# Optimization experiments

Measured on AMD Instinct MI355X. Metric: run time of the kernel, lower is better.

Reference implementation:

```python
import jax, jax.numpy as jnp
import numpy as np

H, E, D, S, B = 16, 1024, 64, 2048, 4  # heads, emb, head_size, seq_len, batch

def setup_inputs() -> dict:
    key = jax.random.key(0)
    ks = jax.random.split(key, 9)
    sc_e = 1.0 / np.sqrt(E)
    sc_hd = 1.0 / np.sqrt(H * D)
    return {
        "x":  jax.random.normal(ks[0], (B, S, E), dtype=jnp.float32),
        # per-head q/k/v projection weights, stacked: [H, E, D]
        "Wq": jax.random.uniform(ks[1], (H, E, D), jnp.float32, -sc_e, sc_e),
        "Wk": jax.random.uniform(ks[2], (H, E, D), jnp.float32, -sc_e, sc_e),
        "Wv": jax.random.uniform(ks[3], (H, E, D), jnp.float32, -sc_e, sc_e),
        "bq": jax.random.uniform(ks[4], (H, D), jnp.float32, -sc_e, sc_e),
        "bk": jax.random.uniform(ks[5], (H, D), jnp.float32, -sc_e, sc_e),
        "bv": jax.random.uniform(ks[6], (H, D), jnp.float32, -sc_e, sc_e),
        # output projection: Linear(H*D -> E)
        "Wo": jax.random.uniform(ks[7], (H * D, E), jnp.float32, -sc_hd, sc_hd),
        "bo": jax.random.uniform(ks[8], (E,), jnp.float32, -sc_hd, sc_hd),
    }

def reference(x, Wq, Wk, Wv, bq, bk, bv, Wo, bo):
    b, s, e = x.shape
    # batched per-head projections: [B, H, S, D]
    q = jnp.einsum("bse,hed->bhsd", x, Wq) + bq[None, :, None, :]
    k = jnp.einsum("bse,hed->bhsd", x, Wk) + bk[None, :, None, :]
    v = jnp.einsum("bse,hed->bhsd", x, Wv) + bv[None, :, None, :]
    scale = 1.0 / jnp.sqrt(jnp.asarray(q.shape[-1], q.dtype))
    scores = jnp.einsum("bhqd,bhkd->bhqk", q, k) * scale  # [B,H,S,S]
    causal = jnp.tril(jnp.ones((s, s), dtype=bool))
    scores = jnp.where(causal[None, None], scores, jnp.asarray(-jnp.inf, scores.dtype))
    attn = jax.nn.softmax(scores, axis=-1)
    heads = jnp.einsum("bhqk,bhkd->bhqd", attn, v)  # [B,H,S,D]
    concat = heads.transpose(0, 2, 1, 3).reshape(b, s, -1)  # [B,S,H*D]
    return concat @ Wo + bo  # dropout is identity at inference
```

## Files before the change

### kernel.cpp

```cpp
#include <hip/hip_runtime.h>
#include <hip/hip_bf16.h>

#define H_ 16
#define E_ 1024
#define D_ 64
#define S_ 2048
#define B_ 4
#define M_ (B_ * S_)

typedef __bf16 bf16_t;
typedef __bf16 bf16x8 __attribute__((ext_vector_type(8)));
typedef __bf16 bf16x4 __attribute__((ext_vector_type(4)));
typedef float f32x4 __attribute__((ext_vector_type(4)));

typedef __attribute__((address_space(1))) unsigned int gu32;
typedef __attribute__((address_space(3))) unsigned int lu32;

__device__ __forceinline__ f32x4 mfma16(bf16x8 a, bf16x8 b, f32x4 c) {
  return __builtin_amdgcn_mfma_f32_16x16x32_bf16(a, b, c, 0, 0, 0);
}
__device__ __forceinline__ void gl2lds16(const bf16_t* g, bf16_t* l) {
  __builtin_amdgcn_global_load_lds((const gu32*)g, (lu32*)l, 16, 0, 0);
}

__global__ void detect_k(const unsigned short* __restrict__ x, int* __restrict__ flag) {
  __shared__ int cnt;
  if (threadIdx.x == 0) cnt = 0;
  __syncthreads();
  int hits = 0;
  for (int i = 0; i < 4; ++i) {
    unsigned short v = x[(threadIdx.x * 4 + i) * 2];
    int e = (v >> 7) & 0xFF;
    if (e >= 0xC0) hits++;
  }
  atomicAdd(&cnt, hits);
  __syncthreads();
  if (threadIdx.x == 0) { flag[0] = (cnt > 32) ? 1 : 0; flag[1] = 0; }
}

__global__ __launch_bounds__(256) void convert_x(
    const void* __restrict__ src, bf16_t* __restrict__ dst,
    const int* __restrict__ flag, long n) {
  long i = ((long)blockIdx.x * 256 + threadIdx.x) * 8;
  if (i >= n) return;
  bf16x8 v;
  if (*flag) {
    const float* s = (const float*)src;
    for (int j = 0; j < 8; ++j) v[j] = (bf16_t)s[i + j];
  } else {
    v = *(const bf16x8*)((const bf16_t*)src + i);
  }
  *(bf16x8*)(dst + i) = v;
}

__global__ __launch_bounds__(256) void transpose_k(
    const void* __restrict__ src_, bf16_t* __restrict__ dst,
    const int* __restrict__ flag, int K, int N, long sStride, long dStride) {
  __shared__ __align__(16) bf16_t tile[64][72];
  const int f32 = *flag;
  dst += (long)blockIdx.z * dStride;
  const int tk = blockIdx.x * 64, tn = blockIdx.y * 64;
  const int t = threadIdx.x;
  for (int i = 0; i < 2; ++i) {
    int c = t + i * 256;
    int r = c >> 3, col = (c & 7) * 8;
    if (f32) {
      const float* s = (const float*)src_ + (long)blockIdx.z * sStride;
      const float* p = &s[(long)(tk + r) * N + tn + col];
      for (int j = 0; j < 8; ++j) tile[r][col + j] = (bf16_t)p[j];
    } else {
      const bf16_t* s = (const bf16_t*)src_ + (long)blockIdx.z * sStride;
      *(bf16x8*)&tile[r][col] = *(const bf16x8*)&s[(long)(tk + r) * N + tn + col];
    }
  }
  __syncthreads();
  for (int i = 0; i < 2; ++i) {
    int c = t + i * 256;
    int r = c >> 3, col = (c & 7) * 8;
    bf16x8 v;
    for (int j = 0; j < 8; ++j) v[j] = tile[col + j][r];
    *(bf16x8*)&dst[(long)(tn + r) * K + tk + col] = v;
  }
}

__global__ __launch_bounds__(256) void transpose_qkv(
    const void* __restrict__ s0, const void* __restrict__ s1,
    const void* __restrict__ s2,
    bf16_t* __restrict__ d0, bf16_t* __restrict__ d1, bf16_t* __restrict__ d2,
    const int* __restrict__ flag) {
  __shared__ __align__(16) bf16_t tile[64][72];
  const int f32 = *flag;
  const int which = blockIdx.z >> 4, h = blockIdx.z & 15;
  const void* src_ = which == 0 ? s0 : (which == 1 ? s1 : s2);
  bf16_t* dst = (which == 0 ? d0 : (which == 1 ? d1 : d2)) + (long)h * E_ * D_;
  const long sOff = (long)h * E_ * D_;
  const int tk = blockIdx.x * 64;
  const int t = threadIdx.x;
  for (int i = 0; i < 2; ++i) {
    int c = t + i * 256;
    int r = c >> 3, col = (c & 7) * 8;
    if (f32) {
      const float* s = (const float*)src_ + sOff;
      const float* p = &s[(long)(tk + r) * D_ + col];
      for (int j = 0; j < 8; ++j) tile[r][col + j] = (bf16_t)p[j];
    } else {
      const bf16_t* s = (const bf16_t*)src_ + sOff;
      *(bf16x8*)&tile[r][col] = *(const bf16x8*)&s[(long)(tk + r) * D_ + col];
    }
  }
  __syncthreads();
  for (int i = 0; i < 2; ++i) {
    int c = t + i * 256;
    int r = c >> 3, col = (c & 7) * 8;
    bf16x8 v;
    for (int j = 0; j < 8; ++j) v[j] = tile[col + j][r];
    *(bf16x8*)&dst[(long)r * E_ + tk + col] = v;
  }
}

template <int MODE>
__device__ __forceinline__ void gemm_core(const bf16_t* __restrict__ A,
                                          const bf16_t* __restrict__ Bt,
                                          const void* __restrict__ bias,
                                          void* __restrict__ C, int f32io) {
  constexpr int K = 1024, N = 1024;
  __shared__ __align__(16) bf16_t As[128 * 32];
  __shared__ __align__(16) bf16_t Bs[128 * 32];
  const int t = threadIdx.x;
  const int wave = t >> 6, lane = t & 63;
  const int quad = lane >> 4, l16 = lane & 15;
  const int m0 = blockIdx.x * 128, n0 = blockIdx.y * 128;
  const int wm = (wave & 1) * 64, wn = (wave >> 1) * 64;
  f32x4 acc[4][4] = {};

  for (int kt = 0; kt < K; kt += 32) {
    __syncthreads();
    for (int i = 0; i < 2; ++i) {
      int c = i * 256 + wave * 64 + lane;
      int row = c >> 2, col = (c & 3) << 3;
      const bf16_t* ga;
      if (MODE == 2) {
        int m = m0 + row, kk = kt + col;
        int b = m >> 11, s = m & (S_ - 1);
        int h = kk >> 6, d = kk & 63;
        ga = &A[(((long)(b * H_ + h)) * S_ + s) * D_ + d];
      } else {
        ga = &A[(long)(m0 + row) * K + kt + col];
      }
      gl2lds16(ga, &As[(i * 256 + wave * 64) * 8]);
      gl2lds16(&Bt[(long)(n0 + row) * K + kt + col], &Bs[(i * 256 + wave * 64) * 8]);
    }
    __syncthreads();
    bf16x8 af[4], bfr[4];
    for (int mt = 0; mt < 4; ++mt)
      af[mt] = *(const bf16x8*)&As[(wm + mt * 16 + l16) * 32 + quad * 8];
    for (int nt = 0; nt < 4; ++nt)
      bfr[nt] = *(const bf16x8*)&Bs[(wn + nt * 16 + l16) * 32 + quad * 8];
    for (int mt = 0; mt < 4; ++mt)
      for (int nt = 0; nt < 4; ++nt)
        acc[mt][nt] = mfma16(af[mt], bfr[nt], acc[mt][nt]);
  }
  for (int mt = 0; mt < 4; ++mt) {
    for (int nt = 0; nt < 4; ++nt) {
      int n = n0 + wn + nt * 16 + l16;
      float bv = f32io ? ((const float*)bias)[n] : (float)((const bf16_t*)bias)[n];
      for (int r = 0; r < 4; ++r) {
        int m = m0 + wm + mt * 16 + quad * 4 + r;
        float v = acc[mt][nt][r] + bv;
        if (MODE == 0) {
          int b = m >> 11, s = m & (S_ - 1);
          int h = n >> 6, d = n & 63;
          ((bf16_t*)C)[(((long)(b * H_ + h)) * S_ + s) * D_ + d] = (bf16_t)v;
        } else {
          if (f32io) ((float*)C)[(long)m * N + n] = v;
          else       ((bf16_t*)C)[(long)m * N + n] = (bf16_t)v;
        }
      }
    }
  }
}

__global__ __launch_bounds__(256) void gemm_qkv(
    const bf16_t* __restrict__ A,
    const bf16_t* __restrict__ Bt0, const bf16_t* __restrict__ Bt1,
    const bf16_t* __restrict__ Bt2,
    const void* __restrict__ b0, const void* __restrict__ b1,
    const void* __restrict__ b2,
    bf16_t* __restrict__ C0, bf16_t* __restrict__ C1, bf16_t* __restrict__ C2,
    const int* __restrict__ flag) {
  const int z = blockIdx.z;
  const bf16_t* Bt = z == 0 ? Bt0 : (z == 1 ? Bt1 : Bt2);
  const void* bias = z == 0 ? b0 : (z == 1 ? b1 : b2);
  bf16_t* C = z == 0 ? C0 : (z == 1 ? C1 : C2);
  gemm_core<0>(A, Bt, bias, C, *flag);
}

__global__ __launch_bounds__(256) void gemm_out(
    const bf16_t* __restrict__ A, const bf16_t* __restrict__ Bt,
    const void* __restrict__ bias, void* __restrict__ C,
    const int* __restrict__ flag) {
  gemm_core<2>(A, Bt, bias, C, *flag);
}

__global__ __launch_bounds__(256) void attn_k(
    bf16_t* QO,
    const bf16_t* __restrict__ Kg_,
    const bf16_t* __restrict__ Vtg_) {
  __shared__ __align__(16) bf16_t Ks[64 * 64];
  __shared__ __align__(16) bf16_t Vs[64 * 64];
  __shared__ __align__(16) bf16_t Pq[4][32 * 72];
  const int t = threadIdx.x;
  const int wave = t >> 6, lane = t & 63;
  const int quad = lane >> 4, l16 = lane & 15;
  const int bid = blockIdx.x;
  const int qb = 15 - (bid >> 6);
  const int bh = bid & 63;
  const long base = (long)bh * S_ * D_;
  bf16_t* Qg = QO + base;
  const bf16_t* Kg = Kg_ + base;
  const bf16_t* Vt = Vtg_ + base;
  const int q0 = qb * 128, qrl = wave * 32;
  const int rot = ((lane & 7) - (lane >> 3)) & 7;

  bf16x8 qf[2][2];
  for (int n = 0; n < 2; ++n) {
    long row = q0 + qrl + n * 16 + l16;
    bf16x8 a = *(const bf16x8*)&Qg[row * D_ + quad * 8];
    bf16x8 b = *(const bf16x8*)&Qg[row * D_ + 32 + quad * 8];
    for (int j = 0; j < 8; ++j) {
      a[j] = (bf16_t)((float)a[j] * 0.18033688f);
      b[j] = (bf16_t)((float)b[j] * 0.18033688f);
    }
    qf[n][0] = a; qf[n][1] = b;
  }
  bf16x8 ones;
  for (int j = 0; j < 8; ++j) ones[j] = (bf16_t)1.0f;
  f32x4 o_acc[2][4] = {};
  f32x4 lacc[2] = {};

  const int nkt = 2 * qb + 2;
  for (int kt = 0; kt < nkt; ++kt) {
    __syncthreads();
    for (int i = 0; i < 2; ++i) {
      int c = wave * 2 + i;
      gl2lds16(&Kg[(long)(kt * 64 + c * 8 + (lane >> 3)) * D_ + rot * 8],
               &Ks[c * 512]);
      gl2lds16(&Vt[(long)(c * 8 + (lane >> 3)) * S_ + kt * 64 + rot * 8],
               &Vs[c * 512]);
    }
    __syncthreads();

    if (kt * 64 > q0 + qrl + 31) continue;

    f32x4 sc[2][4];
    for (int mt = 0; mt < 4; ++mt) {
      int krow = mt * 16 + l16;
      bf16x8 kf0 = *(const bf16x8*)&Ks[krow * 64 + (((quad + krow) & 7) << 3)];
      bf16x8 kf1 = *(const bf16x8*)&Ks[krow * 64 + (((quad + 4 + krow) & 7) << 3)];
      for (int n = 0; n < 2; ++n) {
        f32x4 z = {0.f, 0.f, 0.f, 0.f};
        z = mfma16(kf0, qf[n][0], z);
        z = mfma16(kf1, qf[n][1], z);
        sc[n][mt] = z;
      }
    }
    if (kt * 64 + 63 > q0 + qrl) {
      for (int n = 0; n < 2; ++n) {
        int qr = q0 + qrl + n * 16 + l16;
        for (int mt = 0; mt < 4; ++mt)
          for (int r = 0; r < 4; ++r) {
            int kc = kt * 64 + mt * 16 + quad * 4 + r;
            if (kc > qr) sc[n][mt][r] = -1e30f;
          }
      }
    }
    for (int n = 0; n < 2; ++n)
      for (int mt = 0; mt < 4; ++mt) {
        bf16x4 pb;
        for (int r = 0; r < 4; ++r)
          pb[r] = (bf16_t)__builtin_amdgcn_exp2f(sc[n][mt][r]);
        *(bf16x4*)&Pq[wave][(n * 16 + l16) * 72 + mt * 16 + quad * 4] = pb;
      }
    bf16x8 pf[2][2];
    for (int m = 0; m < 2; ++m) {
      pf[m][0] = *(const bf16x8*)&Pq[wave][(m * 16 + l16) * 72 + quad * 8];
      pf[m][1] = *(const bf16x8*)&Pq[wave][(m * 16 + l16) * 72 + 32 + quad * 8];
    }
    for (int m = 0; m < 2; ++m) {
      lacc[m] = mfma16(pf[m][0], ones, lacc[m]);
      lacc[m] = mfma16(pf[m][1], ones, lacc[m]);
    }
    for (int dt = 0; dt < 4; ++dt) {
      int drow = dt * 16 + l16;
      bf16x8 vf0 = *(const bf16x8*)&Vs[drow * 64 + (((quad + drow) & 7) << 3)];
      bf16x8 vf1 = *(const bf16x8*)&Vs[drow * 64 + (((quad + 4 + drow) & 7) << 3)];
      for (int m = 0; m < 2; ++m) {
        o_acc[m][dt] = mfma16(pf[m][0], vf0, o_acc[m][dt]);
        o_acc[m][dt] = mfma16(pf[m][1], vf1, o_acc[m][dt]);
      }
    }
  }
  for (int m = 0; m < 2; ++m)
    for (int r = 0; r < 4; ++r) {
      float inv = 1.0f / lacc[m][r];
      long qg = q0 + qrl + m * 16 + quad * 4 + r;
      for (int dt = 0; dt < 4; ++dt)
        Qg[qg * D_ + dt * 16 + l16] = (bf16_t)(o_acc[m][dt][r] * inv);
    }
}

extern "C" void kernel_launch(void* const* d_in, const int* in_sizes, int n_in,
                              void* d_out, int out_size, void* d_ws, size_t ws_size,
                              hipStream_t stream) {
  (void)in_sizes; (void)n_in; (void)out_size; (void)ws_size;
  const void* x  = d_in[0];
  const void* Wq = d_in[1];
  const void* Wk = d_in[2];
  const void* Wv = d_in[3];
  const void* bq = d_in[4];
  const void* bk = d_in[5];
  const void* bv = d_in[6];
  const void* Wo = d_in[7];
  const void* bo = d_in[8];

  char* base = (char*)d_ws;
  int* flag = (int*)base;
  bf16_t* p = (bf16_t*)(base + 16);
  bf16_t* xb_ = p; p += (size_t)M_ * E_;
  bf16_t* qo_ = p; p += (size_t)B_ * H_ * S_ * D_;
  bf16_t* kb_ = p; p += (size_t)B_ * H_ * S_ * D_;
  bf16_t* vb_ = p; p += (size_t)B_ * H_ * S_ * D_;
  bf16_t* wqt = p; p += (size_t)H_ * D_ * E_;
  bf16_t* wkt = p; p += (size_t)H_ * D_ * E_;
  bf16_t* wvt = p; p += (size_t)H_ * D_ * E_;
  bf16_t* wot = p; p += (size_t)E_ * E_;

  detect_k<<<1, 256, 0, stream>>>((const unsigned short*)x, flag);

  convert_x<<<(M_ * E_) / (256 * 8), 256, 0, stream>>>(x, xb_, flag, (long)M_ * E_);

  transpose_qkv<<<dim3(16, 1, 48), 256, 0, stream>>>(Wq, Wk, Wv, wqt, wkt, wvt, flag);
  transpose_k<<<dim3(16, 16, 1), 256, 0, stream>>>(Wo, wot, flag, E_, E_, 0, 0);

  gemm_qkv<<<dim3(M_ / 128, 8, 3), 256, 0, stream>>>(
      xb_, wqt, wkt, wvt, bq, bk, bv, qo_, kb_, vb_, flag);

  transpose_k<<<dim3(S_ / 64, 1, B_ * H_), 256, 0, stream>>>(
      vb_, xb_, flag + 1, S_, D_, (long)S_ * D_, (long)S_ * D_);

  attn_k<<<dim3(1024), 256, 0, stream>>>(qo_, kb_, xb_);

  gemm_out<<<dim3(M_ / 128, 8, 1), 256, 0, stream>>>(qo_, wot, bo, d_out, flag);
}
```

Measured before the change: 297.9 us.

## Fuse QKV GEMMs to share A tile, swizzle LDS, fold dtype detect into convert

The QKV projection becomes one kernel: each block loads the x tile once and multiplies it against all three weight tiles, so three 4x4 accumulator sets live in registers. This cuts repeated reads of A and the grid size. Both GEMMs now use an XOR swizzle on the LDS column to reduce bank conflicts on fragment reads. The separate dtype-detect kernel is removed; each convert block detects the dtype itself with a wave ballot, which saves one launch. The cost is heavy register pressure (192 accumulator floats) and fewer blocks, which may lower occupancy.

```diff
diff --git a/kernel.cpp b/kernel.cpp
--- a/kernel.cpp
+++ b/kernel.cpp
@@ -23,28 +23,25 @@
   __builtin_amdgcn_global_load_lds((const gu32*)g, (lu32*)l, 16, 0, 0);
 }
 
-__global__ void detect_k(const unsigned short* __restrict__ x, int* __restrict__ flag) {
-  __shared__ int cnt;
-  if (threadIdx.x == 0) cnt = 0;
-  __syncthreads();
-  int hits = 0;
+__device__ __forceinline__ int detect_f32(const unsigned short* __restrict__ xu) {
+  int lane = threadIdx.x & 63;
+  int cnt = 0;
   for (int i = 0; i < 4; ++i) {
-    unsigned short v = x[(threadIdx.x * 4 + i) * 2];
-    int e = (v >> 7) & 0xFF;
-    if (e >= 0xC0) hits++;
-  }
-  atomicAdd(&cnt, hits);
-  __syncthreads();
-  if (threadIdx.x == 0) { flag[0] = (cnt > 32) ? 1 : 0; flag[1] = 0; }
+    unsigned short v = xu[(lane * 4 + i) * 2];
+    cnt += __popcll(__ballot(((v >> 7) & 0xFF) >= 0xC0));
+  }
+  return cnt > 16;
 }
 
 __global__ __launch_bounds__(256) void convert_x(
     const void* __restrict__ src, bf16_t* __restrict__ dst,
-    const int* __restrict__ flag, long n) {
+    int* __restrict__ flag, long n) {
+  const int f32 = detect_f32((const unsigned short*)src);
+  if (blockIdx.x == 0 && threadIdx.x == 0) { flag[0] = f32; flag[1] = 0; }
   long i = ((long)blockIdx.x * 256 + threadIdx.x) * 8;
   if (i >= n) return;
   bf16x8 v;
-  if (*flag) {
+  if (f32) {
     const float* s = (const float*)src;
     for (int j = 0; j < 8; ++j) v[j] = (bf16_t)s[i + j];
   } else {
@@ -118,44 +115,105 @@
   }
 }
 
-template <int MODE>
-__device__ __forceinline__ void gemm_core(const bf16_t* __restrict__ A,
-                                          const bf16_t* __restrict__ Bt,
-                                          const void* __restrict__ bias,
-                                          void* __restrict__ C, int f32io) {
-  constexpr int K = 1024, N = 1024;
+__global__ __launch_bounds__(256) void gemm_qkv3(
+    const bf16_t* __restrict__ A,
+    const bf16_t* __restrict__ Bt0, const bf16_t* __restrict__ Bt1,
+    const bf16_t* __restrict__ Bt2,
+    const void* __restrict__ b0, const void* __restrict__ b1,
+    const void* __restrict__ b2,
+    bf16_t* __restrict__ C0, bf16_t* __restrict__ C1, bf16_t* __restrict__ C2,
+    const int* __restrict__ flag) {
+  constexpr int K = 1024;
   __shared__ __align__(16) bf16_t As[128 * 32];
-  __shared__ __align__(16) bf16_t Bs[128 * 32];
+  __shared__ __align__(16) bf16_t Bs[3][128 * 32];
   const int t = threadIdx.x;
   const int wave = t >> 6, lane = t & 63;
   const int quad = lane >> 4, l16 = lane & 15;
   const int m0 = blockIdx.x * 128, n0 = blockIdx.y * 128;
   const int wm = (wave & 1) * 64, wn = (wave >> 1) * 64;
-  f32x4 acc[4][4] = {};
+  const int swz = (l16 >> 1) & 3;
+  f32x4 acc[3][4][4] = {};
 
   for (int kt = 0; kt < K; kt += 32) {
     __syncthreads();
     for (int i = 0; i < 2; ++i) {
       int c = i * 256 + wave * 64 + lane;
-      int row = c >> 2, col = (c & 3) << 3;
-      const bf16_t* ga;
-      if (MODE == 2) {
-        int m = m0 + row, kk = kt + col;
-        int b = m >> 11, s = m & (S_ - 1);
-        int h = kk >> 6, d = kk & 63;
-        ga = &A[(((long)(b * H_ + h)) * S_ + s) * D_ + d];
-      } else {
-        ga = &A[(long)(m0 + row) * K + kt + col];
-      }
-      gl2lds16(ga, &As[(i * 256 + wave * 64) * 8]);
-      gl2lds16(&Bt[(long)(n0 + row) * K + kt + col], &Bs[(i * 256 + wave * 64) * 8]);
+      int row = c >> 2;
+      int srcc = (c & 3) ^ ((c >> 3) & 3);
+      int dst = (i * 256 + wave * 64) * 8;
+      const long go = (long)(n0 + row) * K + kt + srcc * 8;
+      gl2lds16(&A[(long)(m0 + row) * K + kt + srcc * 8], &As[dst]);
+      gl2lds16(&Bt0[go], &Bs[0][dst]);
+      gl2lds16(&Bt1[go], &Bs[1][dst]);
+      gl2lds16(&Bt2[go], &Bs[2][dst]);
+    }
+    __syncthreads();
+    bf16x8 af[4];
+    for (int mt = 0; mt < 4; ++mt)
+      af[mt] = *(const bf16x8*)&As[(wm + mt * 16 + l16) * 32 + ((quad ^ swz) << 3)];
+    for (int z = 0; z < 3; ++z) {
+      bf16x8 bfr[4];
+      for (int nt = 0; nt < 4; ++nt)
+        bfr[nt] = *(const bf16x8*)&Bs[z][(wn + nt * 16 + l16) * 32 + ((quad ^ swz) << 3)];
+      for (int mt = 0; mt < 4; ++mt)
+        for (int nt = 0; nt < 4; ++nt)
+          acc[z][mt][nt] = mfma16(af[mt], bfr[nt], acc[z][mt][nt]);
+    }
+  }
+  const int f32io = *flag;
+  for (int z = 0; z < 3; ++z) {
+    const void* bz = z == 0 ? b0 : (z == 1 ? b1 : b2);
+    bf16_t* Cz = z == 0 ? C0 : (z == 1 ? C1 : C2);
+    for (int nt = 0; nt < 4; ++nt) {
+      int n = n0 + wn + nt * 16 + l16;
+      float bv = f32io ? ((const float*)bz)[n] : (float)((const bf16_t*)bz)[n];
+      int h = n >> 6, d = n & 63;
+      for (int mt = 0; mt < 4; ++mt)
+        for (int r = 0; r < 4; ++r) {
+          int m = m0 + wm + mt * 16 + quad * 4 + r;
+          int b = m >> 11, s = m & (S_ - 1);
+          Cz[(((long)(b * H_ + h)) * S_ + s) * D_ + d] =
+              (bf16_t)(acc[z][mt][nt][r] + bv);
+        }
+    }
+  }
+}
+
+__global__ __launch_bounds__(256) void gemm_out(
+    const bf16_t* __restrict__ A, const bf16_t* __restrict__ Bt,
+    const void* __restrict__ bias, void* __restrict__ C,
+    const int* __restrict__ flag) {
+  constexpr int K = 1024, N = 1024;
+  __shared__ __align__(16) bf16_t As[128 * 32];
+  __shared__ __align__(16) bf16_t Bs[128 * 32];
+  const int t = threadIdx.x;
+  const int wave = t >> 6, lane = t & 63;
+  const int quad = lane >> 4, l16 = lane & 15;
+  const int m0 = blockIdx.x * 128, n0 = blockIdx.y * 128;
+  const int wm = (wave & 1) * 64, wn = (wave >> 1) * 64;
+  const int swz = (l16 >> 1) & 3;
+  const int f32io = *flag;
+  f32x4 acc[4][4] = {};
+
+  for (int kt = 0; kt < K; kt += 32) {
+    __syncthreads();
+    for (int i = 0; i < 2; ++i) {
+      int c = i * 256 + wave * 64 + lane;
+      int row = c >> 2;
+      int srcc = (c & 3) ^ ((c >> 3) & 3);
+      int dst = (i * 256 + wave * 64) * 8;
+      int m = m0 + row, kk = kt + srcc * 8;
+      int b = m >> 11, s = m & (S_ - 1);
+      int h = kk >> 6, d = kk & 63;
+      gl2lds16(&A[(((long)(b * H_ + h)) * S_ + s) * D_ + d], &As[dst]);
+      gl2lds16(&Bt[(long)(n0 + row) * K + kt + srcc * 8], &Bs[dst]);
     }
     __syncthreads();
     bf16x8 af[4], bfr[4];
     for (int mt = 0; mt < 4; ++mt)
-      af[mt] = *(const bf16x8*)&As[(wm + mt * 16 + l16) * 32 + quad * 8];
+      af[mt] = *(const bf16x8*)&As[(wm + mt * 16 + l16) * 32 + ((quad ^ swz) << 3)];
     for (int nt = 0; nt < 4; ++nt)
-      bfr[nt] = *(const bf16x8*)&Bs[(wn + nt * 16 + l16) * 32 + quad * 8];
+      bfr[nt] = *(const bf16x8*)&Bs[(wn + nt * 16 + l16) * 32 + ((quad ^ swz) << 3)];
     for (int mt = 0; mt < 4; ++mt)
       for (int nt = 0; nt < 4; ++nt)
         acc[mt][nt] = mfma16(af[mt], bfr[nt], acc[mt][nt]);
@@ -167,39 +225,11 @@
       for (int r = 0; r < 4; ++r) {
         int m = m0 + wm + mt * 16 + quad * 4 + r;
         float v = acc[mt][nt][r] + bv;
-        if (MODE == 0) {
-          int b = m >> 11, s = m & (S_ - 1);
-          int h = n >> 6, d = n & 63;
-          ((bf16_t*)C)[(((long)(b * H_ + h)) * S_ + s) * D_ + d] = (bf16_t)v;
-        } else {
-          if (f32io) ((float*)C)[(long)m * N + n] = v;
-          else       ((bf16_t*)C)[(long)m * N + n] = (bf16_t)v;
-        }
-      }
-    }
-  }
-}
-
-__global__ __launch_bounds__(256) void gemm_qkv(
-    const bf16_t* __restrict__ A,
-    const bf16_t* __restrict__ Bt0, const bf16_t* __restrict__ Bt1,
-    const bf16_t* __restrict__ Bt2,
-    const void* __restrict__ b0, const void* __restrict__ b1,
-    const void* __restrict__ b2,
-    bf16_t* __restrict__ C0, bf16_t* __restrict__ C1, bf16_t* __restrict__ C2,
-    const int* __restrict__ flag) {
-  const int z = blockIdx.z;
-  const bf16_t* Bt = z == 0 ? Bt0 : (z == 1 ? Bt1 : Bt2);
-  const void* bias = z == 0 ? b0 : (z == 1 ? b1 : b2);
-  bf16_t* C = z == 0 ? C0 : (z == 1 ? C1 : C2);
-  gemm_core<0>(A, Bt, bias, C, *flag);
-}
-
-__global__ __launch_bounds__(256) void gemm_out(
-    const bf16_t* __restrict__ A, const bf16_t* __restrict__ Bt,
-    const void* __restrict__ bias, void* __restrict__ C,
-    const int* __restrict__ flag) {
-  gemm_core<2>(A, Bt, bias, C, *flag);
+        if (f32io) ((float*)C)[(long)m * N + n] = v;
+        else       ((bf16_t*)C)[(long)m * N + n] = (bf16_t)v;
+      }
+    }
+  }
 }
 
 __global__ __launch_bounds__(256) void attn_k(
@@ -335,14 +365,12 @@
   bf16_t* wvt = p; p += (size_t)H_ * D_ * E_;
   bf16_t* wot = p; p += (size_t)E_ * E_;
 
-  detect_k<<<1, 256, 0, stream>>>((const unsigned short*)x, flag);
-
   convert_x<<<(M_ * E_) / (256 * 8), 256, 0, stream>>>(x, xb_, flag, (long)M_ * E_);
 
   transpose_qkv<<<dim3(16, 1, 48), 256, 0, stream>>>(Wq, Wk, Wv, wqt, wkt, wvt, flag);
   transpose_k<<<dim3(16, 16, 1), 256, 0, stream>>>(Wo, wot, flag, E_, E_, 0, 0);
 
-  gemm_qkv<<<dim3(M_ / 128, 8, 3), 256, 0, stream>>>(
+  gemm_qkv3<<<dim3(M_ / 128, 8), 256, 0, stream>>>(
       xb_, wqt, wkt, wvt, bq, bk, bv, qo_, kb_, vb_, flag);
 
   transpose_k<<<dim3(S_ / 64, 1, B_ * H_), 256, 0, stream>>>(
@@ -350,5 +378,5 @@
 
   attn_k<<<dim3(1024), 256, 0, stream>>>(qo_, kb_, xb_);
 
-  gemm_out<<<dim3(M_ / 128, 8, 1), 256, 0, stream>>>(qo_, wot, bo, d_out, flag);
-}
+  gemm_out<<<dim3(M_ / 128, 8), 256, 0, stream>>>(qo_, wot, bo, d_out, flag);
+}
```

New measurement: 318.5 us. 6.9% more time.
